# Optimization experiments

Measured on AMD Instinct MI355X. Metric: run time of the kernel, lower is better.

The kernel has to match this reference:

```python
import math
import jax, jax.numpy as jnp
import numpy as np
from jax import lax

N, C, H, W = 8, 256, 56, 56
S41, S42, S14 = 1, -1, 1  # fixed values for random roll shifts in original __init__


def setup_inputs() -> dict:
    key = jax.random.key(0)
    ks = jax.random.split(key, 9)
    c8 = C // 8
    x = jax.random.normal(ks[0], (N, C, H, W), jnp.float32)
    p2 = jax.random.normal(ks[1], (1, C, H, W), jnp.float32) * 0.02
    w6 = jax.random.normal(ks[2], (c8, C), jnp.float32) * (1.0 / math.sqrt(C))
    w7 = jax.random.normal(ks[3], (C, 9 * C), jnp.float32) * (1.0 / math.sqrt(9 * C))
    p9 = jax.random.normal(ks[4], (1, c8, H, W), jnp.float32) * 0.02
    b11 = math.sqrt(3.0 / c8)
    p11 = jax.random.uniform(ks[5], (c8, 1), jnp.float32, -b11, b11)
    w12 = jax.random.normal(ks[6], (C, 1, 3, 1), jnp.float32) * (1.0 / math.sqrt(3.0))
    w15 = jax.random.normal(ks[7], (C, C), jnp.float32) * (1.0 / math.sqrt(C))
    b16 = math.sqrt(3.0 / C)
    p16 = jax.random.uniform(ks[8], (C, H * W), jnp.float32, -b16, b16)
    return dict(x=x, p2=p2, w6=w6, w7=w7, p9=p9, p11=p11, w12=w12, w15=w15, p16=p16)


def _unfold33_d3(x):
    # F.unfold(x, (3,3), dilation=(3,3), padding=(3,3)) -> (n, c, 3, 3, h, w)
    xp = jnp.pad(x, ((0, 0), (0, 0), (3, 3), (3, 3)))
    rows = [jnp.stack([xp[:, :, 3 * i:3 * i + H, 3 * j:3 * j + W] for j in range(3)], axis=2)
            for i in range(3)]
    return jnp.stack(rows, axis=2)


def _forward(x, p2, w6, w7, p9, p11, w12, w15, p16):
    n = x.shape[0]
    s_hw = 1.0 / math.sqrt(H * W)
    s_c = 1.0 / math.sqrt(C)
    t1 = _unfold33_d3(x)                                    # n,c,3,3,h,w
    t2 = p2 * x
    t3 = t2 * t2
    t4 = jnp.roll(jnp.roll(t3, S41, axis=2), S42, axis=3)
    t5 = jax.nn.softmax(t4, axis=2)                          # softmax over h
    t6 = jnp.einsum('nchw,oc->nohw', t3, w6)                 # 1x1 conv c -> c//8
    t7 = jnp.einsum('nkhw,ok->nohw', t1.reshape(n, 9 * C, H, W), w7)  # 1x1 conv 9c -> c
    t8 = jnp.einsum('ncs,nds->ncd', t5.reshape(n, C, H * W), t3.reshape(n, C, H * W)) * s_hw
    t9 = p9 * t6
    t10 = jnp.maximum(t5, t7)
    t11 = jnp.einsum('nbhw,be->nehw', t9, p11)[:, 0]         # (n,h,w)
    # depthwise conv, kernel (3,1), dilation (2,1), padding (2,0)
    t12 = lax.conv_general_dilated(t10, w12, window_strides=(1, 1),
                                   padding=((2, 2), (0, 0)), rhs_dilation=(2, 1),
                                   feature_group_count=C,
                                   dimension_numbers=('NCHW', 'OIHW', 'NCHW'))
    t13 = t11[:, None] - t12                                 # (n,c,h,w)
    t14 = jnp.roll(x, S14, axis=2)
    t15 = jnp.einsum('nchw,oc->nohw', t14, w15)              # 1x1 conv c -> c
    t16 = jnp.einsum('nbc,bd->ndc', t8, p16)                 # (n, hw, c)
    t17 = t3 - t15
    t18 = t7 * t17
    t19 = jnp.einsum('ncs,nsd->ncd', t17.reshape(n, C, H * W), t16) * s_hw  # (n,c,c)
    t20 = (jnp.einsum('ndc,nds->ncs', t19, t13.reshape(n, C, H * W)) * s_c).reshape(n, C, H, W)
    return t20 + t18


def reference(x, p2, w6, w7, p9, p11, w12, w15, p16):
    return _forward(x, p2, w6, w7, p9, p11, w12, w15, p16)
```

## Files before the change

kernel.cpp:

```cpp
#include <hip/hip_runtime.h>

#define Nn 8
#define Cc 256
#define C8 32
#define Hh 56
#define Ww 56
#define HW 3136
#define CHW (Cc * HW)
#define K9C 2304
#define S_HW (1.0f / 56.0f)
#define S_C  0.0625f
#define XPLANE 3844
#define XPAD_ELEMS (Nn * XPLANE * Cc)

typedef float f4 __attribute__((ext_vector_type(4)));
typedef unsigned short ushort;
typedef __attribute__((ext_vector_type(4))) unsigned short u16x4;
typedef __attribute__((ext_vector_type(8))) unsigned short u16x8;
typedef __attribute__((ext_vector_type(8))) short short8;
typedef __attribute__((ext_vector_type(4))) float floatx4;

__device__ __forceinline__ ushort f2bf(float f) {
    union { float f; unsigned u; } v; v.f = f;
    unsigned r = v.u + 0x7FFF + ((v.u >> 16) & 1);
    return (ushort)(r >> 16);
}
__device__ __forceinline__ float bf2f(ushort u) {
    union { unsigned u; float f; } v; v.u = ((unsigned)u) << 16;
    return v.f;
}

__global__ __launch_bounds__(256) void k_t3sm(const float* __restrict__ x,
                                              const float* __restrict__ p2,
                                              ushort* __restrict__ t3b,
                                              ushort* __restrict__ t5b) {
    __shared__ float ld[HW];
    __shared__ float mx[Ww], rs[Ww];
    int tid = threadIdx.x;
    int nc = blockIdx.x;
    int c = nc & 255;
    const float* xn = x + (size_t)nc * HW;
    const float* pp = p2 + (size_t)c * HW;
    ushort* t3n = t3b + (size_t)nc * HW;
    for (int i = tid; i < 784; i += 256) {
        f4 xv = *(const f4*)(xn + i * 4);
        f4 pv = *(const f4*)(pp + i * 4);
        f4 t = xv * pv;
        f4 q = t * t;
        *(f4*)(&ld[i * 4]) = q;
        u16x4 qb = { f2bf(q[0]), f2bf(q[1]), f2bf(q[2]), f2bf(q[3]) };
        *(u16x4*)(t3n + i * 4) = qb;
    }
    __syncthreads();
    if (tid < Ww) {
        float m = -1e30f;
        for (int h = 0; h < Hh; h++) m = fmaxf(m, ld[h * Ww + tid]);
        float s = 0.f;
        for (int h = 0; h < Hh; h++) s += __expf(ld[h * Ww + tid] - m);
        mx[tid] = m;
        rs[tid] = 1.0f / s;
    }
    __syncthreads();
    ushort* dst = t5b + (size_t)nc * HW;
    for (int i = tid; i < HW; i += 256) {
        int h = i / Ww, w = i - h * Ww;
        int wp = (w + 1 == Ww) ? 0 : w + 1;
        int hp = (h == 0) ? Hh - 1 : h - 1;
        dst[i] = f2bf(__expf(ld[hp * Ww + wp] - mx[wp]) * rs[wp]);
    }
}

__global__ __launch_bounds__(256) void k_xT(const float* __restrict__ x,
                                            ushort* __restrict__ xpT) {
    __shared__ ushort Ts[112][40];
    int tid = threadIdx.x;
    int n = blockIdx.z;
    int c0 = blockIdx.y * 32;
    int s0 = blockIdx.x * 112;
    const float* xn = x + (size_t)n * CHW;
#pragma unroll
    for (int e = 0; e < 4; e++) {
        int lin = tid + e * 256;
        int sq = lin & 31;
        int c_l = lin >> 5;
        if (sq < 28) {
            f4 v = *(const f4*)(xn + (size_t)(c0 + c_l) * HW + s0 + sq * 4);
#pragma unroll
            for (int k = 0; k < 4; k++) Ts[sq * 4 + k][c_l] = f2bf(v[k]);
        }
    }
    __syncthreads();
    ushort* dstn = xpT + (size_t)n * (XPLANE * Cc);
#pragma unroll
    for (int e = 0; e < 2; e++) {
        int lin = tid + e * 256;
        int r = lin >> 2, ch = lin & 3;
        if (r < 112) {
            u16x8 v = *(const u16x8*)(&Ts[r][ch * 8]);
            int s_g = s0 + r;
            int h = s_g / 56;
            int wc = s_g - h * 56;
            size_t drow = (size_t)((h + 3) * 62 + wc + 3);
            *(u16x8*)(dstn + drow * Cc + c0 + ch * 8) = v;
        }
    }
}

__global__ __launch_bounds__(256) void k_w7p(const float* __restrict__ w7,
                                             ushort* __restrict__ w7p) {
    int g = blockIdx.x * 256 + threadIdx.x;
    int ij = g >> 16;
    int rem = g & 65535;
    int o = rem >> 8;
    int c = rem & 255;
    w7p[g] = f2bf(w7[(size_t)o * K9C + c * 9 + ij]);
}

__global__ __launch_bounds__(256) void k_cvt(const float* __restrict__ src,
                                             ushort* __restrict__ dst) {
    int g = blockIdx.x * 256 + threadIdx.x;
    dst[g] = f2bf(src[g]);
}

__global__ __launch_bounds__(256, 3) void k_gemm_t7_mfma(
        const ushort* __restrict__ xpT,
        const ushort* __restrict__ w7p,
        ushort* __restrict__ t7b) {
    __shared__ __align__(16) ushort Bs[620][40];
    int tid = threadIdx.x;
    int lane = tid & 63;
    int ln15 = lane & 15, quad = lane >> 4;
    int wave = tid >> 6;
    int wo = (wave >> 1) * 32;
    int wsx = (wave & 1) * 112;
    int n = blockIdx.z;
    int hb = blockIdx.y;
    int o0 = blockIdx.x * 64;
    const ushort* stagePtr = xpT + (size_t)n * (XPLANE * Cc) + (size_t)(hb * 248) * Cc;

    int sp0[7];
#pragma unroll
    for (int f = 0; f < 7; f++) {
        int s_l = wsx + f * 16 + ln15;
        int orow = s_l / 56;
        int wv = s_l - orow * 56;
        sp0[f] = orow * 62 + wv;
    }

    floatx4 acc[2][7] = {};
    u16x8 pre[10];
#pragma unroll
    for (int e = 0; e < 10; e++) {
        int lin = tid + e * 256;
        if (lin < 2480)
            pre[e] = *(const u16x8*)(stagePtr + (size_t)(lin >> 2) * Cc + (lin & 3) * 8);
    }

    for (int ct = 0; ct < Cc; ct += 32) {
#pragma unroll
        for (int e = 0; e < 10; e++) {
            int lin = tid + e * 256;
            if (lin < 2480)
                *(u16x8*)(&Bs[lin >> 2][(lin & 3) * 8]) = pre[e];
        }
        __syncthreads();
        if (ct + 32 < Cc) {
#pragma unroll
            for (int e = 0; e < 10; e++) {
                int lin = tid + e * 256;
                if (lin < 2480)
                    pre[e] = *(const u16x8*)(stagePtr + (size_t)(lin >> 2) * Cc +
                                             ct + 32 + (lin & 3) * 8);
            }
        }
        const ushort* wp = w7p + ct + quad * 8;
#pragma unroll
        for (int ij = 0; ij < 9; ij++) {
            int dsp = (ij / 3) * 186 + (ij % 3) * 3;
            short8 a0 = *(const short8*)(wp + (size_t)(ij * 256 + o0 + wo + ln15) * Cc);
            short8 a1 = *(const short8*)(wp + (size_t)(ij * 256 + o0 + wo + 16 + ln15) * Cc);
#pragma unroll
            for (int f = 0; f < 7; f++) {
                short8 b = *(const short8*)(&Bs[sp0[f] + dsp][quad * 8]);
                acc[0][f] = __builtin_amdgcn_mfma_f32_16x16x32_bf16(a0, b, acc[0][f], 0, 0, 0);
                acc[1][f] = __builtin_amdgcn_mfma_f32_16x16x32_bf16(a1, b, acc[1][f], 0, 0, 0);
            }
        }
        __syncthreads();
    }

    ushort* t7n = t7b + (size_t)n * CHW;
    int sBase = hb * 224 + wsx;
#pragma unroll
    for (int m = 0; m < 2; m++) {
        int obase = o0 + wo + m * 16 + quad * 4;
#pragma unroll
        for (int f = 0; f < 7; f++) {
            int s = sBase + f * 16 + ln15;
#pragma unroll
            for (int r = 0; r < 4; r++)
                t7n[(size_t)(obase + r) * HW + s] = f2bf(acc[m][f][r]);
        }
    }
}

__global__ __launch_bounds__(256) void k_gemm_t15_mfma(const ushort* __restrict__ xpT,
                                                       const ushort* __restrict__ w15b,
                                                       const ushort* __restrict__ t3b,
                                                       ushort* __restrict__ t17b) {
    __shared__ __align__(16) ushort As[128][40];
    __shared__ __align__(16) ushort Bs[128][40];
    int tid = threadIdx.x;
    int lane = tid & 63;
    int ln15 = lane & 15;
    int quad = lane >> 4;
    int wave = tid >> 6;
    int wm64 = (wave >> 1) * 64;
    int wn64 = (wave & 1) * 64;
    int n = blockIdx.z;
    int s0 = blockIdx.x * 128;
    int o0 = blockIdx.y * 128;
    const ushort* xT = xpT + (size_t)n * (XPLANE * Cc);

    int sp_src[2];
#pragma unroll
    for (int e = 0; e < 2; e++) {
        int s_l = (tid + e * 256) >> 2;
        int s = s0 + s_l;
        int sc = s < HW ? s : HW - 1;
        int h = sc / Ww, w = sc - h * Ww;
        int hp = (h == 0) ? 58 : h + 2;
        sp_src[e] = hp * 62 + w + 3;
    }
    int chq = (tid & 3) * 8;

    floatx4 acc[4][4] = {};

    for (int kt = 0; kt < Cc; kt += 32) {
#pragma unroll
        for (int e = 0; e < 2; e++) {
            int lin = tid + e * 256;
            int m = lin >> 2, kq = (lin & 3) * 8;
            *(u16x8*)(&As[m][kq]) =
                *(const u16x8*)(w15b + (size_t)(o0 + m) * Cc + kt + kq);
        }
#pragma unroll
        for (int e = 0; e < 2; e++) {
            int s_l = (tid + e * 256) >> 2;
            *(u16x8*)(&Bs[s_l][chq]) =
                *(const u16x8*)(xT + (size_t)sp_src[e] * Cc + kt + chq);
        }
        __syncthreads();

        short8 af[4], bf[4];
#pragma unroll
        for (int a = 0; a < 4; a++)
            af[a] = *(const short8*)(&As[wm64 + a * 16 + ln15][quad * 8]);
#pragma unroll
        for (int b = 0; b < 4; b++)
            bf[b] = *(const short8*)(&Bs[wn64 + b * 16 + ln15][quad * 8]);
#pragma unroll
        for (int a = 0; a < 4; a++)
#pragma unroll
            for (int b = 0; b < 4; b++)
                acc[a][b] = __builtin_amdgcn_mfma_f32_16x16x32_bf16(
                    af[a], bf[b], acc[a][b], 0, 0, 0);
        __syncthreads();
    }

    const ushort* t3n = t3b + (size_t)n * CHW;
    ushort* t17n = t17b + (size_t)n * CHW;
#pragma unroll
    for (int a = 0; a < 4; a++) {
        int obase = o0 + wm64 + a * 16 + quad * 4;
#pragma unroll
        for (int b = 0; b < 4; b++) {
            int s = s0 + wn64 + b * 16 + ln15;
            if (s < HW) {
#pragma unroll
                for (int r = 0; r < 4; r++) {
                    size_t idx = (size_t)(obase + r) * HW + s;
                    t17n[idx] = f2bf(bf2f(t3n[idx]) - acc[a][b][r]);
                }
            }
        }
    }
}

__global__ __launch_bounds__(256) void k_abt2(const ushort* __restrict__ t5b,
                                              const ushort* __restrict__ t3b,
                                              const ushort* __restrict__ t17b,
                                              const ushort* __restrict__ p16b,
                                              float* __restrict__ t8,
                                              float* __restrict__ uu) {
    __shared__ __align__(16) ushort As[128][40];
    __shared__ __align__(16) ushort Bs[128][40];
    int tid = threadIdx.x;
    int lane = tid & 63;
    int ln15 = lane & 15;
    int quad = lane >> 4;
    int wave = tid >> 6;
    int wm64 = (wave >> 1) * 64;
    int wn64 = (wave & 1) * 64;
    int sel = blockIdx.y >> 1;
    int c0 = (blockIdx.y & 1) * 128;
    int d0 = blockIdx.x * 128;
    int z = blockIdx.z;
    int n = z / 7, ks = z - n * 7;
    const ushort* An = (sel ? t17b : t5b) + (size_t)n * CHW;
    const ushort* Bb = sel ? p16b : (t3b + (size_t)n * CHW);
    float* outp = (sel ? uu : t8) + (size_t)n * (Cc * Cc);
    float scale = sel ? 1.0f : S_HW;

    floatx4 acc[4][4] = {};
    int kbeg = ks * 448;

    for (int kt = kbeg; kt < kbeg + 448; kt += 32) {
#pragma unroll
        for (int e = 0; e < 2; e++) {
            int lin = tid + e * 256;
            int m = lin >> 2, kq = (lin & 3) * 8;
            *(u16x8*)(&As[m][kq]) =
                *(const u16x8*)(An + (size_t)(c0 + m) * HW + kt + kq);
            *(u16x8*)(&Bs[m][kq]) =
                *(const u16x8*)(Bb + (size_t)(d0 + m) * HW + kt + kq);
        }
        __syncthreads();

        short8 af[4], bf[4];
#pragma unroll
        for (int a = 0; a < 4; a++)
            af[a] = *(const short8*)(&As[wm64 + a * 16 + ln15][quad * 8]);
#pragma unroll
        for (int b = 0; b < 4; b++)
            bf[b] = *(const short8*)(&Bs[wn64 + b * 16 + ln15][quad * 8]);
#pragma unroll
        for (int a = 0; a < 4; a++)
#pragma unroll
            for (int b = 0; b < 4; b++)
                acc[a][b] = __builtin_amdgcn_mfma_f32_16x16x32_bf16(
                    af[a], bf[b], acc[a][b], 0, 0, 0);
        __syncthreads();
    }

#pragma unroll
    for (int a = 0; a < 4; a++) {
        int cbase = c0 + wm64 + a * 16 + quad * 4;
#pragma unroll
        for (int b = 0; b < 4; b++) {
            int d = d0 + wn64 + b * 16 + ln15;
#pragma unroll
            for (int r = 0; r < 4; r++)
                atomicAdd(&outp[(size_t)(cbase + r) * Cc + d], acc[a][b][r] * scale);
        }
    }
}

__global__ __launch_bounds__(256) void k_gemm_t19(const float* __restrict__ u,
                                                  const float* __restrict__ t8,
                                                  ushort* __restrict__ t19Tb) {
    __shared__ float As[64][20];
    __shared__ float Bs[16][68];
    int tid = threadIdx.x;
    int tx = tid & 15, ty = tid >> 4;
    int n = blockIdx.z;
    int d0 = blockIdx.x * 64;
    int c0 = blockIdx.y * 64;
    const float* un = u + (size_t)n * Cc * Cc;
    const float* t8n = t8 + (size_t)n * Cc * Cc;
    f4 acc[4] = {};
    for (int kt = 0; kt < Cc; kt += 16) {
        int lin = tid * 4;
        {
            int r = lin >> 4, kq = lin & 15;
            *(f4*)(&As[r][kq]) = *(const f4*)(un + (size_t)(c0 + r) * Cc + kt + kq);
        }
        {
            int kk = lin >> 6, col = lin & 63;
            *(f4*)(&Bs[kk][col]) = *(const f4*)(t8n + (size_t)(kt + kk) * Cc + d0 + col);
        }
        __syncthreads();
#pragma unroll
        for (int kk = 0; kk < 16; kk += 4) {
            f4 av[4], bv[4];
#pragma unroll
            for (int a = 0; a < 4; a++) av[a] = *(const f4*)(&As[ty * 4 + a][kk]);
#pragma unroll
            for (int q = 0; q < 4; q++) bv[q] = *(const f4*)(&Bs[kk + q][tx * 4]);
#pragma unroll
            for (int a = 0; a < 4; a++)
#pragma unroll
                for (int q = 0; q < 4; q++) acc[a] += av[a][q] * bv[q];
        }
        __syncthreads();
    }
    ushort* on = t19Tb + (size_t)n * Cc * Cc;
#pragma unroll
    for (int a = 0; a < 4; a++) {
        int c = c0 + ty * 4 + a;
#pragma unroll
        for (int j = 0; j < 4; j++)
            on[(size_t)(d0 + tx * 4 + j) * Cc + c] = f2bf(acc[a][j] * S_HW);
    }
}

__global__ __launch_bounds__(256) void k_t11(const ushort* __restrict__ t3b,
                                             const float* __restrict__ w6,
                                             const float* __restrict__ p9,
                                             const float* __restrict__ p11,
                                             float* __restrict__ t11) {
    __shared__ float smem[8704];
    float* w6s = smem;
    float* part = smem;
    float* part2 = smem + 8448;
    int tid = threadIdx.x;
    for (int i = tid; i < C8 * Cc; i += 256) w6s[i] = w6[i];
    __syncthreads();
    int n = blockIdx.y;
    int sl = tid & 63;
    int cg = tid >> 6;
    int s = blockIdx.x * 64 + sl;
    const ushort* t3n = t3b + (size_t)n * CHW + s;
    float acc[C8] = {};
    for (int c = cg * 64; c < cg * 64 + 64; c += 4) {
        float v0 = bf2f(t3n[(c + 0) * HW]);
        float v1 = bf2f(t3n[(c + 1) * HW]);
        float v2 = bf2f(t3n[(c + 2) * HW]);
        float v3 = bf2f(t3n[(c + 3) * HW]);
#pragma unroll
        for (int b = 0; b < C8; b++) {
            f4 wv = *(const f4*)(&w6s[b * Cc + c]);
            acc[b] += wv[0] * v0 + wv[1] * v1 + wv[2] * v2 + wv[3] * v3;
        }
    }
    __syncthreads();
#pragma unroll
    for (int b = 0; b < C8; b++) part[(cg * 64 + sl) * 33 + b] = acc[b];
    __syncthreads();
    float r = 0.f;
#pragma unroll
    for (int j = 0; j < 8; j++) {
        int b = cg * 8 + j;
        float sum = part[(0 * 64 + sl) * 33 + b] + part[(1 * 64 + sl) * 33 + b] +
                    part[(2 * 64 + sl) * 33 + b] + part[(3 * 64 + sl) * 33 + b];
        r += p11[b] * p9[b * HW + s] * sum;
    }
    part2[cg * 64 + sl] = r;
    __syncthreads();
    if (tid < 64)
        t11[(size_t)n * HW + s] = part2[sl] + part2[64 + sl] + part2[128 + sl] + part2[192 + sl];
}

__global__ __launch_bounds__(256) void k_t13(const ushort* __restrict__ t5b,
                                             const ushort* __restrict__ t7b,
                                             const float* __restrict__ t11,
                                             const float* __restrict__ w12,
                                             ushort* __restrict__ t13b) {
    int g = blockIdx.x * 256 + threadIdx.x;
    int idx = g * 4;
    int nc = idx / HW;
    int s = idx - nc * HW;
    int c = nc & 255;
    int n = nc >> 8;
    int h = s / Ww, w = s - h * Ww;
    f4 sum = {0.f, 0.f, 0.f, 0.f};
#pragma unroll
    for (int kh = 0; kh < 3; kh++) {
        int hh = h - 2 + 2 * kh;
        if ((unsigned)hh < (unsigned)Hh) {
            size_t base = (size_t)nc * HW + hh * Ww + w;
            u16x4 t5v = *(const u16x4*)(t5b + base);
            u16x4 t7v = *(const u16x4*)(t7b + base);
            float wk = w12[c * 3 + kh];
#pragma unroll
            for (int j = 0; j < 4; j++)
                sum[j] += wk * fmaxf(bf2f(t5v[j]), bf2f(t7v[j]));
        }
    }
    f4 t11v = *(const f4*)(t11 + (size_t)n * HW + s);
    u16x4 o = { f2bf(t11v[0] - sum[0]), f2bf(t11v[1] - sum[1]),
                f2bf(t11v[2] - sum[2]), f2bf(t11v[3] - sum[3]) };
    *(u16x4*)(t13b + idx) = o;
}

__global__ __launch_bounds__(256) void k_gemm_out_mfma(const ushort* __restrict__ t19Tb,
                                                       const ushort* __restrict__ t13b,
                                                       const ushort* __restrict__ t7b,
                                                       const ushort* __restrict__ t17b,
                                                       float* __restrict__ outp) {
    __shared__ __align__(16) ushort As[128][40];
    __shared__ __align__(16) ushort Bs[128][40];
    int tid = threadIdx.x;
    int lane = tid & 63;
    int ln15 = lane & 15;
    int quad = lane >> 4;
    int wave = tid >> 6;
    int wm64 = (wave >> 1) * 64;
    int wn64 = (wave & 1) * 64;
    int n = blockIdx.z;
    int s0 = blockIdx.x * 128;
    int c0 = blockIdx.y * 128;
    const ushort* An = t19Tb + (size_t)n * Cc * Cc;
    const ushort* t13n = t13b + (size_t)n * CHW;

    floatx4 acc[4][4] = {};

    for (int kt = 0; kt < Cc; kt += 32) {
#pragma unroll
        for (int e = 0; e < 2; e++) {
            int lin = tid + e * 256;
            int m = lin >> 2, kq = (lin & 3) * 8;
            *(u16x8*)(&As[m][kq]) =
                *(const u16x8*)(An + (size_t)(c0 + m) * Cc + kt + kq);
        }
#pragma unroll
        for (int e = 0; e < 2; e++) {
            int lin = tid + e * 256;
            int d_l = lin >> 4;
            int s8 = (lin & 15) * 8;
            int s = s0 + s8;
            int sc = s <= HW - 8 ? s : HW - 8;
            u16x8 v = *(const u16x8*)(t13n + (size_t)(kt + d_l) * HW + sc);
#pragma unroll
            for (int j = 0; j < 8; j++) Bs[s8 + j][d_l] = v[j];
        }
        __syncthreads();

        short8 af[4], bf[4];
#pragma unroll
        for (int a = 0; a < 4; a++)
            af[a] = *(const short8*)(&As[wm64 + a * 16 + ln15][quad * 8]);
#pragma unroll
        for (int b = 0; b < 4; b++)
            bf[b] = *(const short8*)(&Bs[wn64 + b * 16 + ln15][quad * 8]);
#pragma unroll
        for (int a = 0; a < 4; a++)
#pragma unroll
            for (int b = 0; b < 4; b++)
                acc[a][b] = __builtin_amdgcn_mfma_f32_16x16x32_bf16(
                    af[a], bf[b], acc[a][b], 0, 0, 0);
        __syncthreads();
    }

    const ushort* t7n = t7b + (size_t)n * CHW;
    const ushort* t17n = t17b + (size_t)n * CHW;
    float* on = outp + (size_t)n * CHW;
#pragma unroll
    for (int a = 0; a < 4; a++) {
        int cbase = c0 + wm64 + a * 16 + quad * 4;
#pragma unroll
        for (int b = 0; b < 4; b++) {
            int s = s0 + wn64 + b * 16 + ln15;
            if (s < HW) {
#pragma unroll
                for (int r = 0; r < 4; r++) {
                    size_t idx = (size_t)(cbase + r) * HW + s;
                    on[idx] = acc[a][b][r] * S_C + bf2f(t7n[idx]) * bf2f(t17n[idx]);
                }
            }
        }
    }
}

extern "C" void kernel_launch(void* const* d_in, const int* in_sizes, int n_in,
                              void* d_out, int out_size, void* d_ws, size_t ws_size,
                              hipStream_t stream) {
    const float* x   = (const float*)d_in[0];
    const float* p2  = (const float*)d_in[1];
    const float* w6  = (const float*)d_in[2];
    const float* w7  = (const float*)d_in[3];
    const float* p9  = (const float*)d_in[4];
    const float* p11 = (const float*)d_in[5];
    const float* w12 = (const float*)d_in[6];
    const float* w15 = (const float*)d_in[7];
    const float* p16 = (const float*)d_in[8];
    float* ws = (float*)d_ws;

    float* t8  = ws;
    float* uu  = ws + 524288;
    float* t11 = ws + 1048576;
    ushort* ub  = (ushort*)(ws + 1081344);
    ushort* t5b   = ub;
    ushort* t3b   = ub + 6422528;
    ushort* t17b  = ub + 12845056;
    ushort* t13b  = ub + 19267584;
    ushort* t7b   = ub + 25690112;
    ushort* xpT   = ub + 32112640;
    ushort* w7p   = ub + 39985152;
    ushort* w15b  = ub + 40574976;
    ushort* p16b  = ub + 40640512;
    ushort* t19Tb = ub + 41443328;
    float* outp = (float*)d_out;

    hipMemsetAsync(xpT, 0, (size_t)XPAD_ELEMS * 2, stream);
    k_t3sm<<<dim3(Nn * Cc), dim3(256), 0, stream>>>(x, p2, t3b, t5b);
    k_xT<<<dim3(28, 8, Nn), dim3(256), 0, stream>>>(x, xpT);
    k_w7p<<<dim3(2304), dim3(256), 0, stream>>>(w7, w7p);
    k_cvt<<<dim3(256),  dim3(256), 0, stream>>>(w15, w15b);
    k_cvt<<<dim3(3136), dim3(256), 0, stream>>>(p16, p16b);
    hipMemsetAsync(t8, 0, (size_t)Nn * Cc * Cc * 4, stream);
    hipMemsetAsync(uu, 0, (size_t)Nn * Cc * Cc * 4, stream);
    k_gemm_t7_mfma<<<dim3(4, 14, Nn), dim3(256), 0, stream>>>(xpT, w7p, t7b);
    k_gemm_t15_mfma<<<dim3(25, 2, Nn), dim3(256), 0, stream>>>(xpT, w15b, t3b, t17b);
    k_abt2<<<dim3(2, 4, Nn * 7), dim3(256), 0, stream>>>(t5b, t3b, t17b, p16b, t8, uu);
    k_t11<<<dim3(49, Nn), dim3(256), 0, stream>>>(t3b, w6, p9, p11, t11);
    k_gemm_t19<<<dim3(4, 4, Nn), dim3(256), 0, stream>>>(uu, t8, t19Tb);
    k_t13<<<dim3(6272), dim3(256), 0, stream>>>(t5b, t7b, t11, w12, t13b);
    k_gemm_out_mfma<<<dim3(25, 2, Nn), dim3(256), 0, stream>>>(t19Tb, t13b, t7b, t17b, outp);
}
```

Baseline: 361.6 us.

## Merge weight-conversion kernels and swizzle t7 GEMM shared tile with A prefetch

```diff
diff --git a/kernel.cpp b/kernel.cpp
--- a/kernel.cpp
+++ b/kernel.cpp
@@ -106,27 +106,33 @@
     }
 }
 
-__global__ __launch_bounds__(256) void k_w7p(const float* __restrict__ w7,
-                                             ushort* __restrict__ w7p) {
+__global__ __launch_bounds__(256) void k_prep(const float* __restrict__ w7,
+                                              const float* __restrict__ w15,
+                                              const float* __restrict__ p16,
+                                              ushort* __restrict__ w7p,
+                                              ushort* __restrict__ w15b,
+                                              ushort* __restrict__ p16b) {
     int g = blockIdx.x * 256 + threadIdx.x;
-    int ij = g >> 16;
-    int rem = g & 65535;
-    int o = rem >> 8;
-    int c = rem & 255;
-    w7p[g] = f2bf(w7[(size_t)o * K9C + c * 9 + ij]);
-}
-
-__global__ __launch_bounds__(256) void k_cvt(const float* __restrict__ src,
-                                             ushort* __restrict__ dst) {
-    int g = blockIdx.x * 256 + threadIdx.x;
-    dst[g] = f2bf(src[g]);
+    if (g < 589824) {
+        int ij = g >> 16;
+        int rem = g & 65535;
+        int o = rem >> 8;
+        int c = rem & 255;
+        w7p[g] = f2bf(w7[(size_t)o * K9C + c * 9 + ij]);
+    } else if (g < 655360) {
+        int i = g - 589824;
+        w15b[i] = f2bf(w15[i]);
+    } else {
+        int i = g - 655360;
+        if (i < 802816) p16b[i] = f2bf(p16[i]);
+    }
 }
 
 __global__ __launch_bounds__(256, 3) void k_gemm_t7_mfma(
         const ushort* __restrict__ xpT,
         const ushort* __restrict__ w7p,
         ushort* __restrict__ t7b) {
-    __shared__ __align__(16) ushort Bs[620][40];
+    __shared__ __align__(16) ushort Bs[620 * 32];
     int tid = threadIdx.x;
     int lane = tid & 63;
     int ln15 = lane & 15, quad = lane >> 4;
@@ -147,47 +153,47 @@
         sp0[f] = orow * 62 + wv;
     }
 
+    const ushort* wbase = w7p + (size_t)(o0 + wo + ln15) * Cc + quad * 8;
+#define ALOAD(ij, ct, m) (*(const short8*)(wbase + (size_t)(ij) * (256 * Cc) + (m) * (16 * Cc) + (ct)))
+
     floatx4 acc[2][7] = {};
-    u16x8 pre[10];
-#pragma unroll
-    for (int e = 0; e < 10; e++) {
-        int lin = tid + e * 256;
-        if (lin < 2480)
-            pre[e] = *(const u16x8*)(stagePtr + (size_t)(lin >> 2) * Cc + (lin & 3) * 8);
-    }
+    short8 ca0 = ALOAD(0, 0, 0);
+    short8 ca1 = ALOAD(0, 0, 1);
 
     for (int ct = 0; ct < Cc; ct += 32) {
+        __syncthreads();
 #pragma unroll
         for (int e = 0; e < 10; e++) {
             int lin = tid + e * 256;
-            if (lin < 2480)
-                *(u16x8*)(&Bs[lin >> 2][(lin & 3) * 8]) = pre[e];
-        }
-        __syncthreads();
-        if (ct + 32 < Cc) {
-#pragma unroll
-            for (int e = 0; e < 10; e++) {
-                int lin = tid + e * 256;
-                if (lin < 2480)
-                    pre[e] = *(const u16x8*)(stagePtr + (size_t)(lin >> 2) * Cc +
-                                             ct + 32 + (lin & 3) * 8);
+            if (lin < 2480) {
+                int row = lin >> 2, ch = lin & 3;
+                u16x8 v = *(const u16x8*)(stagePtr + (size_t)row * Cc + ct + ch * 8);
+                *(u16x8*)(&Bs[row * 32 + ((ch ^ ((row >> 1) & 3)) << 3)]) = v;
             }
         }
-        const ushort* wp = w7p + ct + quad * 8;
+        __syncthreads();
 #pragma unroll
         for (int ij = 0; ij < 9; ij++) {
             int dsp = (ij / 3) * 186 + (ij % 3) * 3;
-            short8 a0 = *(const short8*)(wp + (size_t)(ij * 256 + o0 + wo + ln15) * Cc);
-            short8 a1 = *(const short8*)(wp + (size_t)(ij * 256 + o0 + wo + 16 + ln15) * Cc);
+            short8 na0, na1;
+            if (!(ij == 8 && ct == Cc - 32)) {
+                int nij = (ij == 8) ? 0 : ij + 1;
+                int nct = (ij == 8) ? ct + 32 : ct;
+                na0 = ALOAD(nij, nct, 0);
+                na1 = ALOAD(nij, nct, 1);
+            }
 #pragma unroll
             for (int f = 0; f < 7; f++) {
-                short8 b = *(const short8*)(&Bs[sp0[f] + dsp][quad * 8]);
-                acc[0][f] = __builtin_amdgcn_mfma_f32_16x16x32_bf16(a0, b, acc[0][f], 0, 0, 0);
-                acc[1][f] = __builtin_amdgcn_mfma_f32_16x16x32_bf16(a1, b, acc[1][f], 0, 0, 0);
+                int r = sp0[f] + dsp;
+                short8 b = *(const short8*)(&Bs[r * 32 + ((quad ^ ((r >> 1) & 3)) << 3)]);
+                acc[0][f] = __builtin_amdgcn_mfma_f32_16x16x32_bf16(ca0, b, acc[0][f], 0, 0, 0);
+                acc[1][f] = __builtin_amdgcn_mfma_f32_16x16x32_bf16(ca1, b, acc[1][f], 0, 0, 0);
             }
-        }
-        __syncthreads();
-    }
+            ca0 = na0;
+            ca1 = na1;
+        }
+    }
+#undef ALOAD
 
     ushort* t7n = t7b + (size_t)n * CHW;
     int sBase = hb * 224 + wsx;
@@ -595,9 +601,7 @@
     hipMemsetAsync(xpT, 0, (size_t)XPAD_ELEMS * 2, stream);
     k_t3sm<<<dim3(Nn * Cc), dim3(256), 0, stream>>>(x, p2, t3b, t5b);
     k_xT<<<dim3(28, 8, Nn), dim3(256), 0, stream>>>(x, xpT);
-    k_w7p<<<dim3(2304), dim3(256), 0, stream>>>(w7, w7p);
-    k_cvt<<<dim3(256),  dim3(256), 0, stream>>>(w15, w15b);
-    k_cvt<<<dim3(3136), dim3(256), 0, stream>>>(p16, p16b);
+    k_prep<<<dim3(5696), dim3(256), 0, stream>>>(w7, w15, p16, w7p, w15b, p16b);
     hipMemsetAsync(t8, 0, (size_t)Nn * Cc * Cc * 4, stream);
     hipMemsetAsync(uu, 0, (size_t)Nn * Cc * Cc * 4, stream);
     k_gemm_t7_mfma<<<dim3(4, 14, Nn), dim3(256), 0, stream>>>(xpT, w7p, t7b);
```

Measured after the change: 384.0 us. +6.2%, slower.
